# Kernel tuning notes

Measured on AMD Instinct MI355X. Metric: run time of the kernel, lower is better.

The kernel has to match this reference:

```python
import jax, jax.numpy as jnp
import numpy as np

L, B, I, H = 1024, 128, 256, 512

def setup_inputs() -> dict:
    key = jax.random.key(0)
    k1, k2, k3, k4, k5 = jax.random.split(key, 5)
    s_i = 1.0 / np.sqrt(I)
    s_h = 1.0 / np.sqrt(H)
    return {
        "x": jax.random.normal(k1, (L, B, I), dtype=jnp.float32),
        "h": jax.random.normal(k2, (B, H), dtype=jnp.float32),
        "Wx": jax.random.uniform(k3, (H, I), jnp.float32, -s_i, s_i),
        "Wh": jax.random.uniform(k4, (H, H), jnp.float32, -s_h, s_h),
        "bh": jax.random.uniform(k5, (H,), jnp.float32, -s_h, s_h),
    }

def reference(x, h, Wx, Wh, bh):
    # Precompute input projection for all timesteps as one big GEMM:
    # (L,B,I) @ (I,H) -> (L,B,H)
    xproj = jnp.einsum("lbi,hi->lbh", x, Wx)

    def step(h_prev, xp_t):
        h_new = jnp.tanh(xp_t + h_prev @ Wh.T + bh)  # (B,H)
        return h_new, h_new

    _, h_seq = jax.lax.scan(step, h, xproj)
    return h_seq  # (L, B, H)
```

## Files before the change

### kernel.cpp

```cpp
#include <hip/hip_runtime.h>

#define L_DIM 1024
#define B_DIM 128
#define I_DIM 256
#define H_DIM 512

typedef unsigned short u16x8 __attribute__((ext_vector_type(8)));
typedef __bf16 bf16x8 __attribute__((ext_vector_type(8)));
typedef float f32x4 __attribute__((ext_vector_type(4)));
typedef unsigned long long u64;
typedef unsigned int u32;

static __device__ __forceinline__ unsigned short f2bf(float f) {
  unsigned u = __builtin_bit_cast(unsigned, f);
  u += 0x7FFFu + ((u >> 16) & 1u);
  return (unsigned short)(u >> 16);
}
static __device__ __forceinline__ float bf2f(unsigned short b) {
  return __builtin_bit_cast(float, ((unsigned)b) << 16);
}
static __device__ __forceinline__ bf16x8 ld_frag_g(const unsigned short* p, size_t idx8) {
  return __builtin_bit_cast(bf16x8, reinterpret_cast<const u16x8*>(p)[idx8]);
}

__global__ void pack_weights(const float* __restrict__ Wx, const float* __restrict__ Wh,
                             unsigned short* __restrict__ WxHi, unsigned short* __restrict__ WxLo,
                             unsigned short* __restrict__ WhHi, unsigned short* __restrict__ WhLo) {
  int tid = blockIdx.x * blockDim.x + threadIdx.x;
  if (tid < 32 * 8 * 64) {
    int lane = tid & 63, kt = (tid >> 6) & 7, nt = tid >> 9;
    int n = nt * 16 + (lane & 15), k0 = kt * 32 + (lane >> 4) * 8;
    const float* src = Wx + (size_t)n * I_DIM + k0;
    #pragma unroll
    for (int j = 0; j < 8; ++j) {
      float v = src[j];
      unsigned short hb = f2bf(v);
      WxHi[(size_t)tid * 8 + j] = hb;
      WxLo[(size_t)tid * 8 + j] = f2bf(v - bf2f(hb));
    }
  }
  if (tid < 32 * 16 * 64) {
    int lane = tid & 63, kt = (tid >> 6) & 15, nt = tid >> 10;
    int n = nt * 16 + (lane & 15), k0 = kt * 32 + (lane >> 4) * 8;
    const float* src = Wh + (size_t)n * H_DIM + k0;
    #pragma unroll
    for (int j = 0; j < 8; ++j) {
      float v = src[j];
      unsigned short hb = f2bf(v);
      WhHi[(size_t)tid * 8 + j] = hb;
      WhLo[(size_t)tid * 8 + j] = f2bf(v - bf2f(hb));
    }
  }
}

__global__ __launch_bounds__(256) void xproj_kernel(const float* __restrict__ x,
    const unsigned short* __restrict__ WxHi, const unsigned short* __restrict__ WxLo,
    const float* __restrict__ bh, float* __restrict__ out) {
  __shared__ unsigned short ahi[128][40];
  __shared__ unsigned short alo[128][40];
  const int tid = threadIdx.x, lane = tid & 63, wid = tid >> 6;
  const int mbase = blockIdx.x * 128, cbase = blockIdx.y * 128;
  const int wrow = (wid >> 1) * 64, wcol = (wid & 1) * 64;
  f32x4 acc[4][4] = {};
  const int srow = tid >> 1, shalf = (tid & 1) * 16;

  for (int kt = 0; kt < 8; ++kt) {
    const f32x4* src = reinterpret_cast<const f32x4*>(
        x + (size_t)(mbase + srow) * I_DIM + kt * 32 + shalf);
    f32x4 v[4];
    v[0] = src[0]; v[1] = src[1]; v[2] = src[2]; v[3] = src[3];
    u16x8 hh[2], ll[2];
    #pragma unroll
    for (int q = 0; q < 2; ++q) {
      #pragma unroll
      for (int e = 0; e < 8; ++e) {
        float f = v[q * 2 + (e >> 2)][e & 3];
        unsigned short hb = f2bf(f);
        hh[q][e] = hb;
        ll[q][e] = f2bf(f - bf2f(hb));
      }
    }
    __syncthreads();
    *reinterpret_cast<u16x8*>(&ahi[srow][shalf]) = hh[0];
    *reinterpret_cast<u16x8*>(&ahi[srow][shalf + 8]) = hh[1];
    *reinterpret_cast<u16x8*>(&alo[srow][shalf]) = ll[0];
    *reinterpret_cast<u16x8*>(&alo[srow][shalf + 8]) = ll[1];
    __syncthreads();

    bf16x8 amh[4], aml[4];
    #pragma unroll
    for (int m = 0; m < 4; ++m) {
      amh[m] = __builtin_bit_cast(bf16x8, *reinterpret_cast<const u16x8*>(
          &ahi[wrow + m * 16 + (lane & 15)][(lane >> 4) * 8]));
      aml[m] = __builtin_bit_cast(bf16x8, *reinterpret_cast<const u16x8*>(
          &alo[wrow + m * 16 + (lane & 15)][(lane >> 4) * 8]));
    }
    bf16x8 bhh[4], bll[4];
    #pragma unroll
    for (int n = 0; n < 4; ++n) {
      int ntg = (cbase + wcol) / 16 + n;
      size_t idx = (size_t)(ntg * 8 + kt) * 64 + lane;
      bhh[n] = ld_frag_g(WxHi, idx);
      bll[n] = ld_frag_g(WxLo, idx);
    }
    #pragma unroll
    for (int m = 0; m < 4; ++m) {
      #pragma unroll
      for (int n = 0; n < 4; ++n) {
        acc[m][n] = __builtin_amdgcn_mfma_f32_16x16x32_bf16(amh[m], bhh[n], acc[m][n], 0, 0, 0);
        acc[m][n] = __builtin_amdgcn_mfma_f32_16x16x32_bf16(aml[m], bhh[n], acc[m][n], 0, 0, 0);
        acc[m][n] = __builtin_amdgcn_mfma_f32_16x16x32_bf16(amh[m], bll[n], acc[m][n], 0, 0, 0);
      }
    }
  }

  #pragma unroll
  for (int n = 0; n < 4; ++n) {
    int col = cbase + wcol + n * 16 + (lane & 15);
    float bv = bh[col];
    #pragma unroll
    for (int m = 0; m < 4; ++m) {
      int rg = mbase + wrow + m * 16 + ((lane >> 4) << 2);
      #pragma unroll
      for (int r = 0; r < 4; ++r)
        out[(size_t)(rg + r) * H_DIM + col] = acc[m][n][r] + bv;
    }
  }
}

__global__ __launch_bounds__(256, 1) void rnn_kernel(const float* __restrict__ h0,
    const unsigned short* __restrict__ WhHi, const unsigned short* __restrict__ WhLo,
    unsigned int* __restrict__ tags, u64* __restrict__ gbuf,
    float* __restrict__ out) {
  __shared__ unsigned short hb[2][16 * 520];
  const int tid = threadIdx.x, lane = tid & 63, w = tid >> 6;
  const int g = blockIdx.x & 7, c = blockIdx.x >> 3;

  bf16x8 wfh[16], wfl[16];
  #pragma unroll
  for (int kt = 0; kt < 16; ++kt) {
    size_t idx = (size_t)((c * 4 + w) * 16 + kt) * 64 + lane;
    wfh[kt] = ld_frag_g(WhHi, idx);
    wfl[kt] = ld_frag_g(WhLo, idx);
  }
  for (int i = tid; i < 1024; i += 256) {
    int row = i >> 6, col0 = (i & 63) * 8;
    const f32x4* s = reinterpret_cast<const f32x4*>(h0 + (size_t)(g * 16 + row) * H_DIM + col0);
    f32x4 v0 = s[0], v1 = s[1];
    u16x8 hv;
    #pragma unroll
    for (int e = 0; e < 4; ++e) { hv[e] = f2bf(v0[e]); hv[4 + e] = f2bf(v1[e]); }
    *reinterpret_cast<u16x8*>(&hb[0][row * 520 + col0]) = hv;
  }
  __syncthreads();

  const int arow = lane & 15;
  const int aoff = (lane >> 4) * 8;
  const int drow = (lane >> 4) * 4;
  const int gcol = c * 64 + w * 16 + (lane & 15);
  const int pslot = (w * 16 + (lane & 15)) * 4 + (lane >> 4);
  const int ccol = tid >> 2;
  const int crow0 = (tid & 3) * 4;

  f32x4 xpA, xpB;
  #pragma unroll
  for (int r = 0; r < 4; ++r)
    xpA[r] = out[(size_t)(g * 16 + drow + r) * H_DIM + gcol];
  #pragma unroll
  for (int r = 0; r < 4; ++r)
    xpB[r] = out[(size_t)B_DIM * H_DIM + (size_t)(g * 16 + drow + r) * H_DIM + gcol];

  for (int t = 0; t < L_DIM; ++t) {
    const size_t obase = ((size_t)t * B_DIM + g * 16) * H_DIM;
    const int cur = t & 1;

    bf16x8 af[16];
    #pragma unroll
    for (int kt = 0; kt < 16; ++kt)
      af[kt] = __builtin_bit_cast(bf16x8, *reinterpret_cast<const u16x8*>(
          &hb[cur][arow * 520 + kt * 32 + aoff]));
    f32x4 a0 = {}, a1 = {}, a2 = {}, a3 = {};
    #pragma unroll
    for (int kt = 0; kt < 16; kt += 2) {
      a0 = __builtin_amdgcn_mfma_f32_16x16x32_bf16(af[kt], wfh[kt], a0, 0, 0, 0);
      a1 = __builtin_amdgcn_mfma_f32_16x16x32_bf16(af[kt], wfl[kt], a1, 0, 0, 0);
      a2 = __builtin_amdgcn_mfma_f32_16x16x32_bf16(af[kt + 1], wfh[kt + 1], a2, 0, 0, 0);
      a3 = __builtin_amdgcn_mfma_f32_16x16x32_bf16(af[kt + 1], wfl[kt + 1], a3, 0, 0, 0);
    }

    float hv[4]; unsigned short hu[4];
    #pragma unroll
    for (int r = 0; r < 4; ++r) {
      float z = a0[r] + a1[r] + a2[r] + a3[r] + xpA[r];
      float e = __expf(2.0f * z);
      hv[r] = 1.0f - 2.0f / (e + 1.0f);
      hu[r] = f2bf(hv[r]);
    }

    if (t == L_DIM - 1) {
      #pragma unroll
      for (int r = 0; r < 4; ++r)
        out[obase + (size_t)(drow + r) * H_DIM + gcol] = hv[r];
      break;
    }

    const unsigned step = (unsigned)(t + 1);
    const unsigned buf = step & 1;

    u64 pv = (u64)hu[0] | ((u64)hu[1] << 16) | ((u64)hu[2] << 32) | ((u64)hu[3] << 48);
    __hip_atomic_store(gbuf + (((size_t)(buf * 8 + g) * 8 + c) * 256 + pslot), pv,
                       __ATOMIC_RELAXED, __HIP_MEMORY_SCOPE_AGENT);
    __builtin_amdgcn_sched_barrier(0);
    asm volatile("s_waitcnt vmcnt(0)" ::: "memory");
    __builtin_amdgcn_sched_barrier(0);
    if (lane == 0)
      __hip_atomic_store(tags + ((size_t)((buf * 8 + g) * 8 + c)) * 4 + w,
                         step, __ATOMIC_RELAXED, __HIP_MEMORY_SCOPE_AGENT);

    #pragma unroll
    for (int r = 0; r < 4; ++r)
      hb[buf][(drow + r) * 520 + gcol] = hu[r];

    #pragma unroll
    for (int r = 0; r < 4; ++r)
      out[obase + (size_t)(drow + r) * H_DIM + gcol] = hv[r];
    xpA = xpB;
    {
      const int tn = (t + 2 < L_DIM) ? t + 2 : L_DIM - 1;
      const size_t obn = ((size_t)tn * B_DIM + g * 16) * H_DIM;
      #pragma unroll
      for (int r = 0; r < 4; ++r)
        xpB[r] = out[obn + (size_t)(drow + r) * H_DIM + gcol];
    }

    if (lane < 7) {
      int s = lane + (lane >= c ? 1 : 0);
      const unsigned int* tp = tags + ((size_t)((buf * 8 + g) * 8 + s)) * 4 + w;
      while (__hip_atomic_load(tp, __ATOMIC_RELAXED, __HIP_MEMORY_SCOPE_AGENT) < step) {}
    }
    __builtin_amdgcn_sched_barrier(0);
    u64 pul[7];
    #pragma unroll
    for (int si = 0; si < 7; ++si) {
      int s = si + (si >= c ? 1 : 0);
      pul[si] = __hip_atomic_load(gbuf + (((size_t)(buf * 8 + g) * 8 + s) * 256 + tid),
                                  __ATOMIC_RELAXED, __HIP_MEMORY_SCOPE_AGENT);
    }
    __builtin_amdgcn_sched_barrier(0);
    #pragma unroll
    for (int si = 0; si < 7; ++si) {
      int s = si + (si >= c ? 1 : 0);
      #pragma unroll
      for (int dr = 0; dr < 4; ++dr)
        hb[buf][(crow0 + dr) * 520 + s * 64 + ccol] = (unsigned short)(pul[si] >> (16 * dr));
    }
    __builtin_amdgcn_sched_barrier(0);
    asm volatile("s_waitcnt lgkmcnt(0)" ::: "memory");
    __builtin_amdgcn_sched_barrier(0);
    __builtin_amdgcn_s_barrier();
    __builtin_amdgcn_sched_barrier(0);
  }
}

extern "C" void kernel_launch(void* const* d_in, const int* in_sizes, int n_in,
                              void* d_out, int out_size, void* d_ws, size_t ws_size,
                              hipStream_t stream) {
  (void)in_sizes; (void)n_in; (void)out_size; (void)ws_size;
  const float* x  = (const float*)d_in[0];
  const float* h0 = (const float*)d_in[1];
  const float* Wx = (const float*)d_in[2];
  const float* Wh = (const float*)d_in[3];
  const float* bh = (const float*)d_in[4];
  float* out = (float*)d_out;

  unsigned short* WxHi = (unsigned short*)d_ws;
  unsigned short* WxLo = WxHi + 131072;
  unsigned short* WhHi = WxLo + 131072;
  unsigned short* WhLo = WhHi + 262144;
  unsigned int*   tags = (unsigned int*)((char*)d_ws + 1572864);
  u64*            gbuf = (u64*)((char*)d_ws + 1575936);

  hipMemsetAsync(tags, 0, 2048, stream);

  hipLaunchKernelGGL(pack_weights, dim3(128), dim3(256), 0, stream,
                     Wx, Wh, WxHi, WxLo, WhHi, WhLo);
  hipLaunchKernelGGL(xproj_kernel, dim3(1024, 4), dim3(256), 0, stream,
                     x, WxHi, WxLo, bh, out);
  hipLaunchKernelGGL(rnn_kernel, dim3(64), dim3(256), 0, stream,
                     h0, WhHi, WhLo, tags, gbuf, out);
}
```

Measured before the change: 2.804 ms.

## Have each RNN block process four batch groups to cut block count

Changes the recurrent kernel from 64 blocks, each handling one 16-row batch group, to 16 blocks that each handle four batch groups and keep them in dynamic shared memory. The Wh register fragments are reused across four groups per step, and fewer blocks take part in the cross-block spin-wait exchange. In return, each block's per-step serial work grows fourfold (four MFMA chains, four sets of exchange loads) and it needs 130 KB of LDS.

```diff
diff --git a/kernel.cpp b/kernel.cpp
--- a/kernel.cpp
+++ b/kernel.cpp
@@ -130,11 +130,13 @@
 
 __global__ __launch_bounds__(256, 1) void rnn_kernel(const float* __restrict__ h0,
     const unsigned short* __restrict__ WhHi, const unsigned short* __restrict__ WhLo,
-    unsigned int* __restrict__ tags, u64* __restrict__ gbuf,
+    u32* __restrict__ tags, u64* __restrict__ gbuf,
     float* __restrict__ out) {
-  __shared__ unsigned short hb[2][16 * 520];
+  extern __shared__ __attribute__((aligned(16))) unsigned short hb[];
+  const int HB = 16 * 520;
   const int tid = threadIdx.x, lane = tid & 63, w = tid >> 6;
-  const int g = blockIdx.x & 7, c = blockIdx.x >> 3;
+  const int c = blockIdx.x & 7;
+  const int gh = blockIdx.x >> 3;
 
   bf16x8 wfh[16], wfl[16];
   #pragma unroll
@@ -143,16 +145,6 @@
     wfh[kt] = ld_frag_g(WhHi, idx);
     wfl[kt] = ld_frag_g(WhLo, idx);
   }
-  for (int i = tid; i < 1024; i += 256) {
-    int row = i >> 6, col0 = (i & 63) * 8;
-    const f32x4* s = reinterpret_cast<const f32x4*>(h0 + (size_t)(g * 16 + row) * H_DIM + col0);
-    f32x4 v0 = s[0], v1 = s[1];
-    u16x8 hv;
-    #pragma unroll
-    for (int e = 0; e < 4; ++e) { hv[e] = f2bf(v0[e]); hv[4 + e] = f2bf(v1[e]); }
-    *reinterpret_cast<u16x8*>(&hb[0][row * 520 + col0]) = hv;
-  }
-  __syncthreads();
 
   const int arow = lane & 15;
   const int aoff = (lane >> 4) * 8;
@@ -162,97 +154,130 @@
   const int ccol = tid >> 2;
   const int crow0 = (tid & 3) * 4;
 
-  f32x4 xpA, xpB;
+  {
+    int row = tid >> 4, cb = (tid & 15) * 32;
+    #pragma unroll
+    for (int q = 0; q < 4; ++q) {
+      const f32x4* s = reinterpret_cast<const f32x4*>(
+          h0 + (size_t)((gh * 4 + q) * 16 + row) * H_DIM + cb);
+      #pragma unroll
+      for (int u = 0; u < 4; ++u) {
+        f32x4 v0 = s[2 * u], v1 = s[2 * u + 1];
+        u16x8 hv;
+        #pragma unroll
+        for (int e = 0; e < 4; ++e) { hv[e] = f2bf(v0[e]); hv[4 + e] = f2bf(v1[e]); }
+        *reinterpret_cast<u16x8*>(&hb[(q * 2) * HB + row * 520 + cb + u * 8]) = hv;
+      }
+    }
+  }
+  __syncthreads();
+
+  f32x4 xpA[4], xpB[4];
   #pragma unroll
-  for (int r = 0; r < 4; ++r)
-    xpA[r] = out[(size_t)(g * 16 + drow + r) * H_DIM + gcol];
-  #pragma unroll
-  for (int r = 0; r < 4; ++r)
-    xpB[r] = out[(size_t)B_DIM * H_DIM + (size_t)(g * 16 + drow + r) * H_DIM + gcol];
+  for (int q = 0; q < 4; ++q) {
+    #pragma unroll
+    for (int r = 0; r < 4; ++r) {
+      size_t rw = (size_t)((gh * 4 + q) * 16 + drow + r) * H_DIM + gcol;
+      xpA[q][r] = out[rw];
+      xpB[q][r] = out[(size_t)B_DIM * H_DIM + rw];
+    }
+  }
 
   for (int t = 0; t < L_DIM; ++t) {
-    const size_t obase = ((size_t)t * B_DIM + g * 16) * H_DIM;
-    const int cur = t & 1;
-
-    bf16x8 af[16];
-    #pragma unroll
-    for (int kt = 0; kt < 16; ++kt)
-      af[kt] = __builtin_bit_cast(bf16x8, *reinterpret_cast<const u16x8*>(
-          &hb[cur][arow * 520 + kt * 32 + aoff]));
-    f32x4 a0 = {}, a1 = {}, a2 = {}, a3 = {};
-    #pragma unroll
-    for (int kt = 0; kt < 16; kt += 2) {
-      a0 = __builtin_amdgcn_mfma_f32_16x16x32_bf16(af[kt], wfh[kt], a0, 0, 0, 0);
-      a1 = __builtin_amdgcn_mfma_f32_16x16x32_bf16(af[kt], wfl[kt], a1, 0, 0, 0);
-      a2 = __builtin_amdgcn_mfma_f32_16x16x32_bf16(af[kt + 1], wfh[kt + 1], a2, 0, 0, 0);
-      a3 = __builtin_amdgcn_mfma_f32_16x16x32_bf16(af[kt + 1], wfl[kt + 1], a3, 0, 0, 0);
-    }
-
-    float hv[4]; unsigned short hu[4];
-    #pragma unroll
-    for (int r = 0; r < 4; ++r) {
-      float z = a0[r] + a1[r] + a2[r] + a3[r] + xpA[r];
-      float e = __expf(2.0f * z);
-      hv[r] = 1.0f - 2.0f / (e + 1.0f);
-      hu[r] = f2bf(hv[r]);
-    }
-
-    if (t == L_DIM - 1) {
+    const int cur = t & 1, nxt = cur ^ 1;
+    const unsigned step = (unsigned)(t + 1);
+    const unsigned buf = step & 1;
+
+    #pragma unroll
+    for (int q = 0; q < 4; ++q) {
+      const int g = gh * 4 + q;
+      const unsigned short* hc = hb + (q * 2 + cur) * HB;
+      f32x4 a0 = {}, a1 = {}, a2 = {}, a3 = {};
+      #pragma unroll
+      for (int kt = 0; kt < 16; kt += 2) {
+        bf16x8 af0 = __builtin_bit_cast(bf16x8, *reinterpret_cast<const u16x8*>(
+            &hc[arow * 520 + kt * 32 + aoff]));
+        bf16x8 af1 = __builtin_bit_cast(bf16x8, *reinterpret_cast<const u16x8*>(
+            &hc[arow * 520 + (kt + 1) * 32 + aoff]));
+        a0 = __builtin_amdgcn_mfma_f32_16x16x32_bf16(af0, wfh[kt], a0, 0, 0, 0);
+        a1 = __builtin_amdgcn_mfma_f32_16x16x32_bf16(af0, wfl[kt], a1, 0, 0, 0);
+        a2 = __builtin_amdgcn_mfma_f32_16x16x32_bf16(af1, wfh[kt + 1], a2, 0, 0, 0);
+        a3 = __builtin_amdgcn_mfma_f32_16x16x32_bf16(af1, wfl[kt + 1], a3, 0, 0, 0);
+      }
+      float hv[4]; unsigned short hu[4];
+      #pragma unroll
+      for (int r = 0; r < 4; ++r) {
+        float z = a0[r] + a1[r] + a2[r] + a3[r] + xpA[q][r];
+        float e = __expf(2.0f * z);
+        hv[r] = 1.0f - 2.0f / (e + 1.0f);
+        hu[r] = f2bf(hv[r]);
+      }
+      const size_t obase = ((size_t)t * B_DIM + g * 16) * H_DIM;
       #pragma unroll
       for (int r = 0; r < 4; ++r)
         out[obase + (size_t)(drow + r) * H_DIM + gcol] = hv[r];
-      break;
-    }
-
-    const unsigned step = (unsigned)(t + 1);
-    const unsigned buf = step & 1;
-
-    u64 pv = (u64)hu[0] | ((u64)hu[1] << 16) | ((u64)hu[2] << 32) | ((u64)hu[3] << 48);
-    __hip_atomic_store(gbuf + (((size_t)(buf * 8 + g) * 8 + c) * 256 + pslot), pv,
-                       __ATOMIC_RELAXED, __HIP_MEMORY_SCOPE_AGENT);
+      if (t < L_DIM - 1) {
+        u64 pv = (u64)hu[0] | ((u64)hu[1] << 16) | ((u64)hu[2] << 32) | ((u64)hu[3] << 48);
+        __hip_atomic_store(gbuf + (((size_t)(buf * 8 + g) * 8 + c) * 256 + pslot), pv,
+                           __ATOMIC_RELAXED, __HIP_MEMORY_SCOPE_AGENT);
+        unsigned short* hn = hb + (q * 2 + nxt) * HB;
+        #pragma unroll
+        for (int r = 0; r < 4; ++r)
+          hn[(drow + r) * 520 + gcol] = hu[r];
+      }
+    }
+    if (t == L_DIM - 1) break;
+
     __builtin_amdgcn_sched_barrier(0);
     asm volatile("s_waitcnt vmcnt(0)" ::: "memory");
     __builtin_amdgcn_sched_barrier(0);
-    if (lane == 0)
-      __hip_atomic_store(tags + ((size_t)((buf * 8 + g) * 8 + c)) * 4 + w,
-                         step, __ATOMIC_RELAXED, __HIP_MEMORY_SCOPE_AGENT);
-
-    #pragma unroll
-    for (int r = 0; r < 4; ++r)
-      hb[buf][(drow + r) * 520 + gcol] = hu[r];
-
-    #pragma unroll
-    for (int r = 0; r < 4; ++r)
-      out[obase + (size_t)(drow + r) * H_DIM + gcol] = hv[r];
-    xpA = xpB;
+    if (lane == 0) {
+      #pragma unroll
+      for (int q = 0; q < 4; ++q)
+        __hip_atomic_store(tags + ((size_t)((buf * 8 + gh * 4 + q) * 8 + c)) * 4 + w,
+                           step, __ATOMIC_RELAXED, __HIP_MEMORY_SCOPE_AGENT);
+    }
+
+    #pragma unroll
+    for (int q = 0; q < 4; ++q) xpA[q] = xpB[q];
     {
       const int tn = (t + 2 < L_DIM) ? t + 2 : L_DIM - 1;
-      const size_t obn = ((size_t)tn * B_DIM + g * 16) * H_DIM;
-      #pragma unroll
-      for (int r = 0; r < 4; ++r)
-        xpB[r] = out[obn + (size_t)(drow + r) * H_DIM + gcol];
-    }
-
-    if (lane < 7) {
-      int s = lane + (lane >= c ? 1 : 0);
-      const unsigned int* tp = tags + ((size_t)((buf * 8 + g) * 8 + s)) * 4 + w;
+      #pragma unroll
+      for (int q = 0; q < 4; ++q) {
+        const size_t obn = ((size_t)tn * B_DIM + (gh * 4 + q) * 16) * H_DIM;
+        #pragma unroll
+        for (int r = 0; r < 4; ++r)
+          xpB[q][r] = out[obn + (size_t)(drow + r) * H_DIM + gcol];
+      }
+    }
+
+    if (lane < 28) {
+      int q = lane / 7, si = lane % 7;
+      int s = si + (si >= c ? 1 : 0);
+      const u32* tp = tags + ((size_t)((buf * 8 + gh * 4 + q) * 8 + s)) * 4 + w;
       while (__hip_atomic_load(tp, __ATOMIC_RELAXED, __HIP_MEMORY_SCOPE_AGENT) < step) {}
     }
     __builtin_amdgcn_sched_barrier(0);
-    u64 pul[7];
-    #pragma unroll
-    for (int si = 0; si < 7; ++si) {
-      int s = si + (si >= c ? 1 : 0);
-      pul[si] = __hip_atomic_load(gbuf + (((size_t)(buf * 8 + g) * 8 + s) * 256 + tid),
-                                  __ATOMIC_RELAXED, __HIP_MEMORY_SCOPE_AGENT);
-    }
-    __builtin_amdgcn_sched_barrier(0);
-    #pragma unroll
-    for (int si = 0; si < 7; ++si) {
-      int s = si + (si >= c ? 1 : 0);
-      #pragma unroll
-      for (int dr = 0; dr < 4; ++dr)
-        hb[buf][(crow0 + dr) * 520 + s * 64 + ccol] = (unsigned short)(pul[si] >> (16 * dr));
+    asm volatile("" ::: "memory");
+
+    #pragma unroll
+    for (int q = 0; q < 4; ++q) {
+      const int g = gh * 4 + q;
+      unsigned short* hn = hb + (q * 2 + nxt) * HB;
+      u64 pul[7];
+      #pragma unroll
+      for (int si = 0; si < 7; ++si) {
+        int s = si + (si >= c ? 1 : 0);
+        pul[si] = __hip_atomic_load(gbuf + (((size_t)(buf * 8 + g) * 8 + s) * 256 + tid),
+                                    __ATOMIC_RELAXED, __HIP_MEMORY_SCOPE_AGENT);
+      }
+      #pragma unroll
+      for (int si = 0; si < 7; ++si) {
+        int s = si + (si >= c ? 1 : 0);
+        #pragma unroll
+        for (int dr = 0; dr < 4; ++dr)
+          hn[(crow0 + dr) * 520 + s * 64 + ccol] = (unsigned short)(pul[si] >> (16 * dr));
+      }
     }
     __builtin_amdgcn_sched_barrier(0);
     asm volatile("s_waitcnt lgkmcnt(0)" ::: "memory");
@@ -282,10 +307,13 @@
 
   hipMemsetAsync(tags, 0, 2048, stream);
 
+  hipFuncSetAttribute(reinterpret_cast<const void*>(rnn_kernel),
+                      hipFuncAttributeMaxDynamicSharedMemorySize, 133120);
+
   hipLaunchKernelGGL(pack_weights, dim3(128), dim3(256), 0, stream,
                      Wx, Wh, WxHi, WxLo, WhHi, WhLo);
   hipLaunchKernelGGL(xproj_kernel, dim3(1024, 4), dim3(256), 0, stream,
                      x, WxHi, WxLo, bh, out);
-  hipLaunchKernelGGL(rnn_kernel, dim3(64), dim3(256), 0, stream,
+  hipLaunchKernelGGL(rnn_kernel, dim3(16), dim3(256), 133120, stream,
                      h0, WhHi, WhLo, tags, gbuf, out);
 }
```

Result: slower. 6.890 ms (+145.7%).
